# Kernel optimization log

Measured on AMD Instinct MI355X. Metric: run time of the kernel, lower is better.

Reference implementation:

```python
import jax, jax.numpy as jnp
import numpy as np

NUM_JOINT = 31
BATCH = 131072
# parent index per joint (-1 = root); parents always precede children (topological order)
PARENTS = (-1, 0, 1, 2, 3, 4,
           0, 6, 7, 8, 9,
           0, 11, 12, 13, 14,
           13, 16, 17, 18, 19,
           13, 21, 22, 23, 24,
           13, 26, 27, 28, 29)


def setup_inputs() -> dict:
    key = jax.random.key(0)
    k1, k2, k3, k4 = jax.random.split(key, 4)
    root_position = jax.random.normal(k1, (BATCH, 3), dtype=jnp.float32)
    joint = jax.random.normal(k2, (BATCH, NUM_JOINT * 4), dtype=jnp.float32)
    fake_bone_length = jax.random.uniform(k3, (BATCH, NUM_JOINT), dtype=jnp.float32)
    # skeleton offsets: identity 4x4 with a random bone-offset translation in [:3,3]
    offs = jnp.broadcast_to(jnp.eye(4, dtype=jnp.float32), (NUM_JOINT, 4, 4))
    offs = offs.at[:, :3, 3].set(jax.random.normal(k4, (NUM_JOINT, 3), dtype=jnp.float32))
    return {"root_position": root_position, "joint": joint,
            "fake_bone_length": fake_bone_length, "offsets": offs}


def quaternion_to_matrix(q):
    # q: [..., 4] with (w, x, y, z); pytorch3d-style (normalizes via 2/|q|^2)
    w, x, y, z = q[..., 0], q[..., 1], q[..., 2], q[..., 3]
    two_s = 2.0 / jnp.sum(q * q, axis=-1)
    r00 = 1.0 - two_s * (y * y + z * z)
    r01 = two_s * (x * y - z * w)
    r02 = two_s * (x * z + y * w)
    r10 = two_s * (x * y + z * w)
    r11 = 1.0 - two_s * (x * x + z * z)
    r12 = two_s * (y * z - x * w)
    r20 = two_s * (x * z - y * w)
    r21 = two_s * (y * z + x * w)
    r22 = 1.0 - two_s * (x * x + y * y)
    R = jnp.stack([r00, r01, r02, r10, r11, r12, r20, r21, r22], axis=-1)
    return R.reshape(q.shape[:-1] + (3, 3))


def reference(root_position, joint, fake_bone_length, offsets):
    B = joint.shape[0]
    J = NUM_JOINT
    quats = joint.reshape(B, J, 4)
    R3 = quaternion_to_matrix(quats)                              # [B,J,3,3]
    # embed rotation into homogeneous 4x4
    R4 = jnp.zeros((B, J, 4, 4), dtype=joint.dtype)
    R4 = R4.at[..., :3, :3].set(R3).at[..., 3, 3].set(1.0)
    # offset translation matrices, translation scaled by fake bone length
    trans = offsets[None, :, :3, 3] * fake_bone_length[:, :, None]  # [B,J,3]
    T = jnp.broadcast_to(offsets[None], (B, J, 4, 4)).at[:, :, :3, 3].set(trans)
    RT = jnp.matmul(R4, T)                                        # [B,J,4,4]
    # root translation matrix from root_position * 100
    root_T = jnp.broadcast_to(jnp.eye(4, dtype=joint.dtype), (B, 4, 4))
    root_T = root_T.at[:, :3, 3].set(root_position * 100.0)
    # walk the tree in topological order (fixed small structural loop)
    mats = [None] * J
    mats[0] = jnp.matmul(root_T, RT[:, 0])
    for j in range(1, J):
        mats[j] = jnp.matmul(mats[PARENTS[j]], RT[:, j])
    joint_coordinates = jnp.stack(mats, axis=1)                   # [B,J,4,4]
    # transpose(jc,2,3)[:, j, 3, :] == jc[:, j, :, 3] (homogeneous position column)
    fake_positions = joint_coordinates[:, :, :, 3]                # [B,J,4]
    return fake_positions
```

## Files before the change

### kernel.cpp

```cpp
#include <hip/hip_runtime.h>

constexpr int NJ = 31;
constexpr int ROWS = 16;
constexpr int JF = NJ * 4;

struct M34 {
    float r[9];
    float t[3];
};

__device__ __forceinline__ void make_RT(int j, float4 q, float len,
                                        const float* __restrict__ offs,
                                        float Rr[9], float Rt[3]) {
    const float w = q.x, x = q.y, y = q.z, z = q.w;
    const float two_s = 2.0f / (w * w + x * x + y * y + z * z);
    float R[9];
    R[0] = 1.0f - two_s * (y * y + z * z);
    R[1] = two_s * (x * y - z * w);
    R[2] = two_s * (x * z + y * w);
    R[3] = two_s * (x * y + z * w);
    R[4] = 1.0f - two_s * (x * x + z * z);
    R[5] = two_s * (y * z - x * w);
    R[6] = two_s * (x * z - y * w);
    R[7] = two_s * (y * z + x * w);
    R[8] = 1.0f - two_s * (x * x + y * y);

    const float4* O4 = reinterpret_cast<const float4*>(offs) + (size_t)j * 4;
    const float4 o0 = O4[0], o1 = O4[1], o2 = O4[2];
    const float O[12] = {o0.x, o0.y, o0.z, o1.x, o1.y, o1.z, o2.x, o2.y, o2.z,
                         o0.w * len, o1.w * len, o2.w * len};
#pragma unroll
    for (int r = 0; r < 3; ++r) {
#pragma unroll
        for (int c = 0; c < 3; ++c) {
            Rr[r * 3 + c] = R[r * 3 + 0] * O[0 + c] +
                            R[r * 3 + 1] * O[3 + c] +
                            R[r * 3 + 2] * O[6 + c];
        }
        Rt[r] = R[r * 3 + 0] * O[9] + R[r * 3 + 1] * O[10] + R[r * 3 + 2] * O[11];
    }
}

__device__ __forceinline__ M34 compose(const M34& P, const float Rr[9],
                                       const float Rt[3]) {
    M34 C;
#pragma unroll
    for (int r = 0; r < 3; ++r) {
#pragma unroll
        for (int c = 0; c < 3; ++c) {
            C.r[r * 3 + c] = P.r[r * 3 + 0] * Rr[0 * 3 + c] +
                             P.r[r * 3 + 1] * Rr[1 * 3 + c] +
                             P.r[r * 3 + 2] * Rr[2 * 3 + c];
        }
        C.t[r] = P.r[r * 3 + 0] * Rt[0] + P.r[r * 3 + 1] * Rt[1] +
                 P.r[r * 3 + 2] * Rt[2] + P.t[r];
    }
    return C;
}

__global__ __launch_bounds__(64, 4) void fk_layer_kernel(
    const float* __restrict__ root_position,
    const float* __restrict__ joint,
    const float* __restrict__ fbl,
    const float* __restrict__ offsets,
    float* __restrict__ out) {
    __shared__ float so[ROWS * JF];

    const int lane = threadIdx.x;
    const int r = lane >> 2;
    const int c = lane & 3;
    const int cc = c < 2 ? c : 2;
    const int rowBase = blockIdx.x * ROWS;
    const size_t b = (size_t)(rowBase + r);

    const float4* jq = reinterpret_cast<const float4*>(joint + b * JF);
    float4 q0 = jq[0];
    float4 qa[5], qb[5];
#pragma unroll
    for (int s = 0; s < 5; ++s) qa[s] = jq[1 + 5 * cc + s];
#pragma unroll
    for (int s = 0; s < 5; ++s) qb[s] = jq[16 + 5 * cc + s];

    const float* fr = fbl + b * NJ;
    const float f0 = fr[0];
    float fa[5], fb_[5];
#pragma unroll
    for (int s = 0; s < 5; ++s) fa[s] = fr[1 + 5 * cc + s];
#pragma unroll
    for (int s = 0; s < 5; ++s) fb_[s] = fr[16 + 5 * cc + s];

    const float rx = root_position[b * 3 + 0] * 100.0f;
    const float ry = root_position[b * 3 + 1] * 100.0f;
    const float rz = root_position[b * 3 + 2] * 100.0f;

    float* srow = so + r * JF;

    M34 M0;
    {
        float Rr[9], Rt[3];
        make_RT(0, q0, f0, offsets, Rr, Rt);
#pragma unroll
        for (int i = 0; i < 9; ++i) M0.r[i] = Rr[i];
        M0.t[0] = Rt[0] + rx;
        M0.t[1] = Rt[1] + ry;
        M0.t[2] = Rt[2] + rz;
        if (c == 0)
            *reinterpret_cast<float4*>(&srow[0]) =
                make_float4(M0.t[0], M0.t[1], M0.t[2], 1.0f);
    }

    M34 cur = M0, M13 = M0;
    {
        const int jb = 1 + 5 * cc;
#pragma unroll
        for (int s = 0; s < 5; ++s) {
            const int j = jb + s;
            float Rr[9], Rt[3];
            make_RT(j, qa[s], fa[s], offsets, Rr, Rt);
            cur = compose(cur, Rr, Rt);
            if (c < 3)
                *reinterpret_cast<float4*>(&srow[j * 4]) =
                    make_float4(cur.t[0], cur.t[1], cur.t[2], 1.0f);
            if (s == 2) M13 = cur;
        }
    }

    const int src = (lane & ~3) | 2;
#pragma unroll
    for (int i = 0; i < 9; ++i) M13.r[i] = __shfl(M13.r[i], src, 64);
#pragma unroll
    for (int i = 0; i < 3; ++i) M13.t[i] = __shfl(M13.t[i], src, 64);

    cur = M13;
    {
        const int jb = 16 + 5 * cc;
#pragma unroll
        for (int s = 0; s < 5; ++s) {
            const int j = jb + s;
            float Rr[9], Rt[3];
            make_RT(j, qb[s], fb_[s], offsets, Rr, Rt);
            cur = compose(cur, Rr, Rt);
            if (c < 3)
                *reinterpret_cast<float4*>(&srow[j * 4]) =
                    make_float4(cur.t[0], cur.t[1], cur.t[2], 1.0f);
        }
    }

    __syncthreads();

    const float4* s4 = reinterpret_cast<const float4*>(so);
    float4* gout = reinterpret_cast<float4*>(out + (size_t)rowBase * JF);
#pragma unroll
    for (int ch = 0; ch < 8; ++ch) {
        const int idx = ch * 64 + lane;
        if (idx < ROWS * NJ) gout[idx] = s4[idx];
    }
}

extern "C" void kernel_launch(void* const* d_in, const int* in_sizes, int n_in,
                              void* d_out, int out_size, void* d_ws, size_t ws_size,
                              hipStream_t stream) {
    const float* root = (const float*)d_in[0];
    const float* joint = (const float*)d_in[1];
    const float* fblp = (const float*)d_in[2];
    const float* offs = (const float*)d_in[3];
    float* out = (float*)d_out;

    const int B = in_sizes[0] / 3;
    fk_layer_kernel<<<B / ROWS, 64, 0, stream>>>(root, joint, fblp, offs, out);
}
```

Before: 33.65 us.

## Process four tiles per block with register prefetch of next tile inputs

Each 64-thread block now loops over four row tiles in a grid-stride pattern and loads the next tile's quaternions, bone lengths and root positions into registers while the current tile computes. The __syncthreads is replaced by an lgkmcnt wait, since a single wavefront owns the shared staging buffer. This is meant to hide global load latency and cut block launch count. It raises register pressure from holding two tiles' inputs. The LDS write-after-read ordering across iterations relies on wavefront lockstep.

```diff
diff --git a/kernel.cpp b/kernel.cpp
--- a/kernel.cpp
+++ b/kernel.cpp
@@ -1,12 +1,19 @@
 #include <hip/hip_runtime.h>
 
 constexpr int NJ = 31;
-constexpr int ROWS = 16;
 constexpr int JF = NJ * 4;
+constexpr int RPW = 16;
+constexpr int TILES = 4;
 
 struct M34 {
     float r[9];
     float t[3];
+};
+
+struct Tile {
+    float4 q0, qa[5], qb[5];
+    float f0, fa[5], fb[5];
+    float rx, ry, rz;
 };
 
 __device__ __forceinline__ void make_RT(int j, float4 q, float len,
@@ -58,52 +65,41 @@
     return C;
 }
 
-__global__ __launch_bounds__(64, 4) void fk_layer_kernel(
-    const float* __restrict__ root_position,
-    const float* __restrict__ joint,
-    const float* __restrict__ fbl,
-    const float* __restrict__ offsets,
-    float* __restrict__ out) {
-    __shared__ float so[ROWS * JF];
+__device__ __forceinline__ void load_tile(Tile& T, const float* __restrict__ joint,
+                                          const float* __restrict__ fbl,
+                                          const float* __restrict__ root,
+                                          size_t b, int cc) {
+    const float4* jq = reinterpret_cast<const float4*>(joint + b * JF);
+    T.q0 = jq[0];
+#pragma unroll
+    for (int s = 0; s < 5; ++s) T.qa[s] = jq[1 + 5 * cc + s];
+#pragma unroll
+    for (int s = 0; s < 5; ++s) T.qb[s] = jq[16 + 5 * cc + s];
+    const float* fr = fbl + b * NJ;
+    T.f0 = fr[0];
+#pragma unroll
+    for (int s = 0; s < 5; ++s) T.fa[s] = fr[1 + 5 * cc + s];
+#pragma unroll
+    for (int s = 0; s < 5; ++s) T.fb[s] = fr[16 + 5 * cc + s];
+    T.rx = root[b * 3 + 0] * 100.0f;
+    T.ry = root[b * 3 + 1] * 100.0f;
+    T.rz = root[b * 3 + 2] * 100.0f;
+}
 
-    const int lane = threadIdx.x;
-    const int r = lane >> 2;
-    const int c = lane & 3;
-    const int cc = c < 2 ? c : 2;
-    const int rowBase = blockIdx.x * ROWS;
-    const size_t b = (size_t)(rowBase + r);
-
-    const float4* jq = reinterpret_cast<const float4*>(joint + b * JF);
-    float4 q0 = jq[0];
-    float4 qa[5], qb[5];
-#pragma unroll
-    for (int s = 0; s < 5; ++s) qa[s] = jq[1 + 5 * cc + s];
-#pragma unroll
-    for (int s = 0; s < 5; ++s) qb[s] = jq[16 + 5 * cc + s];
-
-    const float* fr = fbl + b * NJ;
-    const float f0 = fr[0];
-    float fa[5], fb_[5];
-#pragma unroll
-    for (int s = 0; s < 5; ++s) fa[s] = fr[1 + 5 * cc + s];
-#pragma unroll
-    for (int s = 0; s < 5; ++s) fb_[s] = fr[16 + 5 * cc + s];
-
-    const float rx = root_position[b * 3 + 0] * 100.0f;
-    const float ry = root_position[b * 3 + 1] * 100.0f;
-    const float rz = root_position[b * 3 + 2] * 100.0f;
-
+__device__ __forceinline__ void compute_tile(const Tile& T, float* __restrict__ so,
+                                             int r, int c, int cc, int lane,
+                                             const float* __restrict__ offs) {
     float* srow = so + r * JF;
 
     M34 M0;
     {
         float Rr[9], Rt[3];
-        make_RT(0, q0, f0, offsets, Rr, Rt);
+        make_RT(0, T.q0, T.f0, offs, Rr, Rt);
 #pragma unroll
         for (int i = 0; i < 9; ++i) M0.r[i] = Rr[i];
-        M0.t[0] = Rt[0] + rx;
-        M0.t[1] = Rt[1] + ry;
-        M0.t[2] = Rt[2] + rz;
+        M0.t[0] = Rt[0] + T.rx;
+        M0.t[1] = Rt[1] + T.ry;
+        M0.t[2] = Rt[2] + T.rz;
         if (c == 0)
             *reinterpret_cast<float4*>(&srow[0]) =
                 make_float4(M0.t[0], M0.t[1], M0.t[2], 1.0f);
@@ -114,12 +110,11 @@
         const int jb = 1 + 5 * cc;
 #pragma unroll
         for (int s = 0; s < 5; ++s) {
-            const int j = jb + s;
             float Rr[9], Rt[3];
-            make_RT(j, qa[s], fa[s], offsets, Rr, Rt);
+            make_RT(jb + s, T.qa[s], T.fa[s], offs, Rr, Rt);
             cur = compose(cur, Rr, Rt);
             if (c < 3)
-                *reinterpret_cast<float4*>(&srow[j * 4]) =
+                *reinterpret_cast<float4*>(&srow[(jb + s) * 4]) =
                     make_float4(cur.t[0], cur.t[1], cur.t[2], 1.0f);
             if (s == 2) M13 = cur;
         }
@@ -136,24 +131,54 @@
         const int jb = 16 + 5 * cc;
 #pragma unroll
         for (int s = 0; s < 5; ++s) {
-            const int j = jb + s;
             float Rr[9], Rt[3];
-            make_RT(j, qb[s], fb_[s], offsets, Rr, Rt);
+            make_RT(jb + s, T.qb[s], T.fb[s], offs, Rr, Rt);
             cur = compose(cur, Rr, Rt);
             if (c < 3)
-                *reinterpret_cast<float4*>(&srow[j * 4]) =
+                *reinterpret_cast<float4*>(&srow[(jb + s) * 4]) =
                     make_float4(cur.t[0], cur.t[1], cur.t[2], 1.0f);
         }
     }
+}
 
-    __syncthreads();
+__global__ __launch_bounds__(64, 4) void fk_layer_kernel(
+    const float* __restrict__ root_position,
+    const float* __restrict__ joint,
+    const float* __restrict__ fbl,
+    const float* __restrict__ offsets,
+    float* __restrict__ out) {
+    __shared__ float so[RPW * JF];
 
-    const float4* s4 = reinterpret_cast<const float4*>(so);
-    float4* gout = reinterpret_cast<float4*>(out + (size_t)rowBase * JF);
+    const int lane = threadIdx.x;
+    const int r = lane >> 2;
+    const int c = lane & 3;
+    const int cc = c < 2 ? c : 2;
+
+    const int stride = gridDim.x;
+
+    Tile T;
+    load_tile(T, joint, fbl, root_position,
+              (size_t)blockIdx.x * RPW + r, cc);
+
 #pragma unroll
-    for (int ch = 0; ch < 8; ++ch) {
-        const int idx = ch * 64 + lane;
-        if (idx < ROWS * NJ) gout[idx] = s4[idx];
+    for (int k = 0; k < TILES; ++k) {
+        const int tile = blockIdx.x + k * stride;
+
+        compute_tile(T, so, r, c, cc, lane, offsets);
+
+        if (k + 1 < TILES)
+            load_tile(T, joint, fbl, root_position,
+                      (size_t)(tile + stride) * RPW + r, cc);
+
+        asm volatile("s_waitcnt lgkmcnt(0)" ::: "memory");
+
+        const float4* l4 = reinterpret_cast<const float4*>(so);
+        float4* g4 = reinterpret_cast<float4*>(out + (size_t)tile * RPW * JF);
+#pragma unroll
+        for (int ch = 0; ch < 8; ++ch) {
+            const int idx = ch * 64 + lane;
+            if (idx < RPW * NJ) g4[idx] = l4[idx];
+        }
     }
 }
 
@@ -167,5 +192,7 @@
     float* out = (float*)d_out;
 
     const int B = in_sizes[0] / 3;
-    fk_layer_kernel<<<B / ROWS, 64, 0, stream>>>(root, joint, fblp, offs, out);
+    const int tiles = B / RPW;
+    const int blocks = tiles / TILES;
+    fk_layer_kernel<<<blocks, 64, 0, stream>>>(root, joint, fblp, offs, out);
 }
```

Measured after the change: 56.52 us. 67.9% more time.
